# Kernel tuning notes

Measured on AMD Instinct MI355X. Metric: run time of the kernel, lower is better.

The kernel has to match this reference:

```python
import jax, jax.numpy as jnp
import numpy as np

B, T, N, P2, K_S = 8, 64, 128, 256, 64

def setup_inputs() -> dict:
    key = jax.random.key(0)
    k1, k2, k3, k4 = jax.random.split(key, 4)
    x = jax.random.normal(k1, (B, T, N, P2), dtype=jnp.float32)
    W_Q = jax.random.uniform(k2, (P2, K_S), dtype=jnp.float32)
    W_K = jax.random.uniform(k3, (P2, K_S), dtype=jnp.float32)
    W_V = jax.random.uniform(k4, (P2, P2), dtype=jnp.float32)
    return {"x": x, "W_Q": W_Q, "W_K": W_K, "W_V": W_V}

def reference(x, W_Q, W_K, W_V):
    # x: [B, T, N, P2]
    q = jnp.einsum('btnp,pk->btnk', x, W_Q)          # [B,T,N,K_S]
    k = jnp.einsum('btnp,pk->btnk', x, W_K)          # [B,T,N,K_S]
    v = jnp.einsum('btnp,pq->btnq', x, W_V)          # [B,T,N,P2]
    scale = jnp.sqrt(jnp.asarray(K_S, dtype=x.dtype))
    scores = jnp.einsum('btik,btjk->btij', q, k) / scale  # [B,T,N,N]
    # NOTE: original uses nn.Softmax(dim=1) -> softmax over the T axis.
    attn = jax.nn.softmax(scores, axis=1)
    return jnp.einsum('btij,btjq->btiq', attn, v)    # [B,T,N,P2]
```

## Files before the change

### kernel.cpp

```cpp
#include <hip/hip_runtime.h>
#include <hip/hip_bf16.h>

#define Bv 8
#define Tv 64
#define Nv 128
#define P2v 256
#define KSv 64

typedef __attribute__((ext_vector_type(8))) short bf8;
typedef __attribute__((ext_vector_type(4))) float f4;

#define MFMA16(a, b, c) __builtin_amdgcn_mfma_f32_16x16x32_bf16((a), (b), (c), 0, 0, 0)

union B8U {
  bf8 v;
  short s[8];
};

__device__ __forceinline__ unsigned short f2bf(float f) {
  unsigned u = __float_as_uint(f);
  return (unsigned short)((u + 0x7fffu + ((u >> 16) & 1u)) >> 16);
}
__device__ __forceinline__ float bf2f(unsigned short h) {
  return __uint_as_float(((unsigned)h) << 16);
}

__device__ __forceinline__ int qswz(int i, int ks) {
  int gin = ks >> 3;
  return i * 64 + ((gin ^ (i & 7)) << 3) + (ks & 7);
}
__device__ __forceinline__ int vswz(int q, int j) {
  int gin = j >> 3;
  return q * 128 + ((gin ^ (q & 7)) << 3) + (j & 7);
}

__global__ __launch_bounds__(256) void prep_w_kernel(
    const float* __restrict__ Wq, const float* __restrict__ Wk,
    const float* __restrict__ Wv, unsigned short* __restrict__ wqh,
    unsigned short* __restrict__ wql, unsigned short* __restrict__ wkh,
    unsigned short* __restrict__ wkl, unsigned short* __restrict__ wvf) {
  const int e = blockIdx.x * 256 + threadIdx.x;
  if (e < 32768) {
    const float* W = (e < 16384) ? Wq : Wk;
    unsigned short* oh = (e < 16384) ? wqh : wkh;
    unsigned short* ol = (e < 16384) ? wql : wkl;
    const int t = e & 16383;
    const int jj = t & 7, lane = (t >> 3) & 63, nt = (t >> 9) & 3, pt = t >> 11;
    const int p = pt * 32 + 8 * (lane >> 4) + jj;
    const int n = nt * 16 + (lane & 15);
    const float v = W[p * KSv + n];
    const unsigned short h = f2bf(v);
    oh[t] = h;
    ol[t] = f2bf(v - bf2f(h));
  } else {
    const int t = e - 32768;
    const int jj = t & 7, lane = (t >> 3) & 63, nt = (t >> 9) & 15, pt = t >> 13;
    const int p = pt * 32 + 8 * (lane >> 4) + jj;
    const int q = nt * 16 + (lane & 15);
    wvf[t] = f2bf(Wv[p * P2v + q]);
  }
}

__global__ __launch_bounds__(512) void qk_kernel(
    const float* __restrict__ x, const unsigned short* __restrict__ wqh,
    const unsigned short* __restrict__ wql,
    const unsigned short* __restrict__ wkh,
    const unsigned short* __restrict__ wkl, float* __restrict__ S) {
  __shared__ alignas(16) unsigned short qh_l[Nv * KSv];
  __shared__ alignas(16) unsigned short ql_l[Nv * KSv];
  __shared__ alignas(16) unsigned short kh_l[Nv * KSv];
  __shared__ alignas(16) unsigned short kl_l[Nv * KSv];
  const int bt = blockIdx.x;
  const float* __restrict__ X = x + (size_t)bt * (Nv * P2v);
  const int tid = threadIdx.x, lane = tid & 63, wid = tid >> 6;
  const int lg = lane >> 4, lr = lane & 15;
  const int r0 = wid * 16;

  const f4 zero = {0.f, 0.f, 0.f, 0.f};
  f4 aQ[4], aK[4];
#pragma unroll
  for (int n = 0; n < 4; ++n) {
    aQ[n] = zero;
    aK[n] = zero;
  }

  for (int kt = 0; kt < 8; ++kt) {
    const float* xr = X + (r0 + lr) * P2v + kt * 32 + lg * 8;
    const float4 x0 = *(const float4*)(xr);
    const float4 x1 = *(const float4*)(xr + 4);
    const float xs[8] = {x0.x, x0.y, x0.z, x0.w, x1.x, x1.y, x1.z, x1.w};
    B8U xh, xl;
#pragma unroll
    for (int j = 0; j < 8; ++j) {
      const unsigned short h = f2bf(xs[j]);
      xh.s[j] = (short)h;
      xl.s[j] = (short)f2bf(xs[j] - bf2f(h));
    }
#pragma unroll
    for (int n = 0; n < 4; ++n) {
      const int o = ((kt * 4 + n) * 64 + lane) * 8;
      const bf8 fqh = *(const bf8*)(wqh + o);
      const bf8 fql = *(const bf8*)(wql + o);
      const bf8 fkh = *(const bf8*)(wkh + o);
      const bf8 fkl = *(const bf8*)(wkl + o);
      aQ[n] = MFMA16(xh.v, fqh, aQ[n]);
      aQ[n] = MFMA16(xh.v, fql, aQ[n]);
      aQ[n] = MFMA16(xl.v, fqh, aQ[n]);
      aK[n] = MFMA16(xh.v, fkh, aK[n]);
      aK[n] = MFMA16(xh.v, fkl, aK[n]);
      aK[n] = MFMA16(xl.v, fkh, aK[n]);
    }
  }

#pragma unroll
  for (int n = 0; n < 4; ++n) {
#pragma unroll
    for (int r = 0; r < 4; ++r) {
      const int i = r0 + 4 * lg + r;
      const int ks = n * 16 + lr;
      const int off = qswz(i, ks);
      const float qv = aQ[n][r], kv = aK[n][r];
      const unsigned short qh = f2bf(qv), kh = f2bf(kv);
      qh_l[off] = qh;
      ql_l[off] = f2bf(qv - bf2f(qh));
      kh_l[off] = kh;
      kl_l[off] = f2bf(kv - bf2f(kh));
    }
  }
  __syncthreads();

  f4 aS[8];
#pragma unroll
  for (int n = 0; n < 8; ++n) aS[n] = zero;
#pragma unroll
  for (int kt = 0; kt < 2; ++kt) {
    const int qoff = qswz(r0 + lr, kt * 32 + lg * 8);
    const bf8 fqh = *(const bf8*)(qh_l + qoff);
    const bf8 fql = *(const bf8*)(ql_l + qoff);
#pragma unroll
    for (int n = 0; n < 8; ++n) {
      const int koff = qswz(n * 16 + lr, kt * 32 + lg * 8);
      const bf8 fkh = *(const bf8*)(kh_l + koff);
      const bf8 fkl = *(const bf8*)(kl_l + koff);
      aS[n] = MFMA16(fqh, fkh, aS[n]);
      aS[n] = MFMA16(fqh, fkl, aS[n]);
      aS[n] = MFMA16(fql, fkh, aS[n]);
    }
  }
  float* __restrict__ Sb = S + (size_t)bt * (Nv * Nv);
#pragma unroll
  for (int n = 0; n < 8; ++n) {
#pragma unroll
    for (int r = 0; r < 4; ++r) {
      Sb[(r0 + 4 * lg + r) * Nv + n * 16 + lr] = aS[n][r] * 0.125f;
    }
  }
}

__global__ __launch_bounds__(256) void softmax_t_kernel(float* __restrict__ S) {
  const int idx = blockIdx.x * 256 + threadIdx.x;
  const int j = idx & (Nv - 1);
  const int i = (idx >> 7) & (Nv - 1);
  const int b = idx >> 14;
  const size_t base = ((size_t)b * Tv * Nv * Nv) + (size_t)i * Nv + j;

  float vals[Tv];
  float m = -1e30f;
#pragma unroll
  for (int t = 0; t < Tv; ++t) {
    const float v = S[base + (size_t)t * Nv * Nv];
    vals[t] = v;
    m = fmaxf(m, v);
  }
  float s = 0.f;
#pragma unroll
  for (int t = 0; t < Tv; ++t) {
    const float e = __expf(vals[t] - m);
    vals[t] = e;
    s += e;
  }
  const float inv = 1.f / s;
#pragma unroll
  for (int t = 0; t < Tv; ++t) {
    S[base + (size_t)t * Nv * Nv] = vals[t] * inv;
  }
}

__global__ __launch_bounds__(512) void av_kernel(
    const float* __restrict__ x, const unsigned short* __restrict__ wvf,
    const float* __restrict__ A, float* __restrict__ out) {
  __shared__ alignas(16) unsigned short vt[P2v * Nv];
  const int bt = blockIdx.x;
  const float* __restrict__ X = x + (size_t)bt * (Nv * P2v);
  const float* __restrict__ Ab = A + (size_t)bt * (Nv * Nv);
  float* __restrict__ ob = out + (size_t)bt * (Nv * P2v);
  const int tid = threadIdx.x, lane = tid & 63, wid = tid >> 6;
  const int lg = lane >> 4, lr = lane & 15;
  const int r0 = wid * 16;

  const f4 zero = {0.f, 0.f, 0.f, 0.f};
  f4 aV[16];
#pragma unroll
  for (int n = 0; n < 16; ++n) aV[n] = zero;

  for (int kt = 0; kt < 8; ++kt) {
    const float* xr = X + (r0 + lr) * P2v + kt * 32 + lg * 8;
    const float4 x0 = *(const float4*)(xr);
    const float4 x1 = *(const float4*)(xr + 4);
    const float xs[8] = {x0.x, x0.y, x0.z, x0.w, x1.x, x1.y, x1.z, x1.w};
    B8U xh;
#pragma unroll
    for (int j = 0; j < 8; ++j) xh.s[j] = (short)f2bf(xs[j]);
#pragma unroll
    for (int n = 0; n < 16; ++n) {
      const int o = ((kt * 16 + n) * 64 + lane) * 8;
      const bf8 wv = *(const bf8*)(wvf + o);
      aV[n] = MFMA16(xh.v, wv, aV[n]);
    }
  }
#pragma unroll
  for (int n = 0; n < 16; ++n) {
#pragma unroll
    for (int r = 0; r < 4; ++r) {
      const int q = n * 16 + lr;
      const int j = r0 + 4 * lg + r;
      vt[vswz(q, j)] = f2bf(aV[n][r]);
    }
  }
  __syncthreads();

  f4 aO[16];
#pragma unroll
  for (int n = 0; n < 16; ++n) aO[n] = zero;
  for (int kt = 0; kt < 4; ++kt) {
    const float* ar = Ab + (r0 + lr) * Nv + kt * 32 + lg * 8;
    const float4 a0 = *(const float4*)(ar);
    const float4 a1 = *(const float4*)(ar + 4);
    const float as_[8] = {a0.x, a0.y, a0.z, a0.w, a1.x, a1.y, a1.z, a1.w};
    B8U af;
#pragma unroll
    for (int j = 0; j < 8; ++j) af.s[j] = (short)f2bf(as_[j]);
#pragma unroll
    for (int n = 0; n < 16; ++n) {
      const int voff = vswz(n * 16 + lr, kt * 32 + lg * 8);
      const bf8 vf = *(const bf8*)(vt + voff);
      aO[n] = MFMA16(af.v, vf, aO[n]);
    }
  }
#pragma unroll
  for (int n = 0; n < 16; ++n) {
#pragma unroll
    for (int r = 0; r < 4; ++r) {
      ob[(r0 + 4 * lg + r) * P2v + n * 16 + lr] = aO[n][r];
    }
  }
}

extern "C" void kernel_launch(void* const* d_in, const int* in_sizes, int n_in,
                              void* d_out, int out_size, void* d_ws,
                              size_t ws_size, hipStream_t stream) {
  const float* x = (const float*)d_in[0];
  const float* Wq = (const float*)d_in[1];
  const float* Wk = (const float*)d_in[2];
  const float* Wv = (const float*)d_in[3];
  float* out = (float*)d_out;

  unsigned short* wqh = (unsigned short*)d_ws;
  unsigned short* wql = wqh + 16384;
  unsigned short* wkh = wql + 16384;
  unsigned short* wkl = wkh + 16384;
  unsigned short* wvf = wkl + 16384;
  float* S = (float*)((char*)d_ws + 262144);

  hipLaunchKernelGGL(prep_w_kernel, dim3(384), dim3(256), 0, stream, Wq, Wk,
                     Wv, wqh, wql, wkh, wkl, wvf);
  hipLaunchKernelGGL(qk_kernel, dim3(Bv * Tv), dim3(512), 0, stream, x, wqh,
                     wql, wkh, wkl, S);
  hipLaunchKernelGGL(softmax_t_kernel, dim3(Bv * Nv * Nv / 256), dim3(256), 0,
                     stream, S);
  hipLaunchKernelGGL(av_kernel, dim3(Bv * Tv), dim3(512), 0, stream, x, wvf, S,
                     out);
}
```

Baseline: 89.21 us.

## Fuse V projection into QK kernel and stage V through workspace

Adds a qkv_kernel that computes Q, K and V from a single read of x, writing V as transposed bf16 to a workspace buffer. A new av_stage_kernel loads that precomputed V into shared memory instead of recomputing the projection from x. This path runs only when the workspace is large enough; otherwise the old kernels run with partial unrolling and packed ushort4 stores to shared memory. The intent is to avoid reading x twice and to shorten the AV kernel, at the cost of a 32MB V round trip through global memory and higher register pressure in the fused kernel.

Result: slower. 144.9 us (+62.5%).

```diff
diff --git a/kernel.cpp b/kernel.cpp
--- a/kernel.cpp
+++ b/kernel.cpp
@@ -61,6 +61,205 @@
   }
 }
 
+__global__ __launch_bounds__(512) void qkv_kernel(
+    const float* __restrict__ x, const unsigned short* __restrict__ wqh,
+    const unsigned short* __restrict__ wql,
+    const unsigned short* __restrict__ wkh,
+    const unsigned short* __restrict__ wkl,
+    const unsigned short* __restrict__ wvf, float* __restrict__ S,
+    unsigned short* __restrict__ Vt) {
+  __shared__ alignas(16) unsigned short qh_l[Nv * KSv];
+  __shared__ alignas(16) unsigned short ql_l[Nv * KSv];
+  __shared__ alignas(16) unsigned short kh_l[Nv * KSv];
+  __shared__ alignas(16) unsigned short kl_l[Nv * KSv];
+  const int bt = blockIdx.x;
+  const float* __restrict__ X = x + (size_t)bt * (Nv * P2v);
+  const int tid = threadIdx.x, lane = tid & 63, wid = tid >> 6;
+  const int lg = lane >> 4, lr = lane & 15;
+  const int r0 = wid * 16;
+
+  const f4 zero = {0.f, 0.f, 0.f, 0.f};
+  f4 aQ[4], aK[4], aV[16];
+#pragma unroll
+  for (int n = 0; n < 4; ++n) {
+    aQ[n] = zero;
+    aK[n] = zero;
+  }
+#pragma unroll
+  for (int n = 0; n < 16; ++n) aV[n] = zero;
+
+#pragma unroll 2
+  for (int kt = 0; kt < 8; ++kt) {
+    const float* xr = X + (r0 + lr) * P2v + kt * 32 + lg * 8;
+    const float4 x0 = *(const float4*)(xr);
+    const float4 x1 = *(const float4*)(xr + 4);
+    const float xs[8] = {x0.x, x0.y, x0.z, x0.w, x1.x, x1.y, x1.z, x1.w};
+    B8U xh, xl;
+#pragma unroll
+    for (int j = 0; j < 8; ++j) {
+      const unsigned short h = f2bf(xs[j]);
+      xh.s[j] = (short)h;
+      xl.s[j] = (short)f2bf(xs[j] - bf2f(h));
+    }
+#pragma unroll
+    for (int n = 0; n < 4; ++n) {
+      const int o = ((kt * 4 + n) * 64 + lane) * 8;
+      const bf8 fqh = *(const bf8*)(wqh + o);
+      const bf8 fql = *(const bf8*)(wql + o);
+      const bf8 fkh = *(const bf8*)(wkh + o);
+      const bf8 fkl = *(const bf8*)(wkl + o);
+      aQ[n] = MFMA16(xh.v, fqh, aQ[n]);
+      aQ[n] = MFMA16(xh.v, fql, aQ[n]);
+      aQ[n] = MFMA16(xl.v, fqh, aQ[n]);
+      aK[n] = MFMA16(xh.v, fkh, aK[n]);
+      aK[n] = MFMA16(xh.v, fkl, aK[n]);
+      aK[n] = MFMA16(xl.v, fkh, aK[n]);
+    }
+#pragma unroll
+    for (int n = 0; n < 16; ++n) {
+      const int o = ((kt * 16 + n) * 64 + lane) * 8;
+      const bf8 wv = *(const bf8*)(wvf + o);
+      aV[n] = MFMA16(xh.v, wv, aV[n]);
+    }
+  }
+
+  unsigned short* __restrict__ Vtb = Vt + (size_t)bt * (P2v * Nv);
+  const int j0 = r0 + 4 * lg;
+#pragma unroll
+  for (int n = 0; n < 16; ++n) {
+    const int q = n * 16 + lr;
+    ushort4 pk;
+    pk.x = f2bf(aV[n][0]);
+    pk.y = f2bf(aV[n][1]);
+    pk.z = f2bf(aV[n][2]);
+    pk.w = f2bf(aV[n][3]);
+    *(ushort4*)(Vtb + q * Nv + j0) = pk;
+  }
+
+#pragma unroll
+  for (int n = 0; n < 4; ++n) {
+#pragma unroll
+    for (int r = 0; r < 4; ++r) {
+      const int i = r0 + 4 * lg + r;
+      const int ks = n * 16 + lr;
+      const int off = qswz(i, ks);
+      const float qv = aQ[n][r], kv = aK[n][r];
+      const unsigned short qh = f2bf(qv), kh = f2bf(kv);
+      qh_l[off] = qh;
+      ql_l[off] = f2bf(qv - bf2f(qh));
+      kh_l[off] = kh;
+      kl_l[off] = f2bf(kv - bf2f(kh));
+    }
+  }
+  __syncthreads();
+
+  f4 aS[8];
+#pragma unroll
+  for (int n = 0; n < 8; ++n) aS[n] = zero;
+#pragma unroll
+  for (int kt = 0; kt < 2; ++kt) {
+    const int qoff = qswz(r0 + lr, kt * 32 + lg * 8);
+    const bf8 fqh = *(const bf8*)(qh_l + qoff);
+    const bf8 fql = *(const bf8*)(ql_l + qoff);
+#pragma unroll
+    for (int n = 0; n < 8; ++n) {
+      const int koff = qswz(n * 16 + lr, kt * 32 + lg * 8);
+      const bf8 fkh = *(const bf8*)(kh_l + koff);
+      const bf8 fkl = *(const bf8*)(kl_l + koff);
+      aS[n] = MFMA16(fqh, fkh, aS[n]);
+      aS[n] = MFMA16(fqh, fkl, aS[n]);
+      aS[n] = MFMA16(fql, fkh, aS[n]);
+    }
+  }
+  float* __restrict__ Sb = S + (size_t)bt * (Nv * Nv);
+#pragma unroll
+  for (int n = 0; n < 8; ++n) {
+#pragma unroll
+    for (int r = 0; r < 4; ++r) {
+      Sb[(r0 + 4 * lg + r) * Nv + n * 16 + lr] = aS[n][r] * 0.125f;
+    }
+  }
+}
+
+__global__ __launch_bounds__(256) void softmax_t_kernel(float* __restrict__ S) {
+  const int idx = blockIdx.x * 256 + threadIdx.x;
+  const int j = idx & (Nv - 1);
+  const int i = (idx >> 7) & (Nv - 1);
+  const int b = idx >> 14;
+  const size_t base = ((size_t)b * Tv * Nv * Nv) + (size_t)i * Nv + j;
+
+  float vals[Tv];
+  float m = -1e30f;
+#pragma unroll
+  for (int t = 0; t < Tv; ++t) {
+    const float v = S[base + (size_t)t * Nv * Nv];
+    vals[t] = v;
+    m = fmaxf(m, v);
+  }
+  float s = 0.f;
+#pragma unroll
+  for (int t = 0; t < Tv; ++t) {
+    const float e = __expf(vals[t] - m);
+    vals[t] = e;
+    s += e;
+  }
+  const float inv = 1.f / s;
+#pragma unroll
+  for (int t = 0; t < Tv; ++t) {
+    S[base + (size_t)t * Nv * Nv] = vals[t] * inv;
+  }
+}
+
+__global__ __launch_bounds__(512) void av_stage_kernel(
+    const float* __restrict__ A, const unsigned short* __restrict__ Vt,
+    float* __restrict__ out) {
+  __shared__ alignas(16) unsigned short vt[P2v * Nv];
+  const int bt = blockIdx.x;
+  const float* __restrict__ Ab = A + (size_t)bt * (Nv * Nv);
+  const unsigned short* __restrict__ Vtb = Vt + (size_t)bt * (P2v * Nv);
+  float* __restrict__ ob = out + (size_t)bt * (Nv * P2v);
+  const int tid = threadIdx.x, lane = tid & 63, wid = tid >> 6;
+  const int lg = lane >> 4, lr = lane & 15;
+  const int r0 = wid * 16;
+
+#pragma unroll
+  for (int it = 0; it < 8; ++it) {
+    const int c = it * 512 + tid;
+    const int q = c >> 4, gin = c & 15;
+    const uint4 v = *(const uint4*)(Vtb + c * 8);
+    *(uint4*)(vt + q * Nv + ((gin ^ (q & 7)) << 3)) = v;
+  }
+  __syncthreads();
+
+  const f4 zero = {0.f, 0.f, 0.f, 0.f};
+  f4 aO[16];
+#pragma unroll
+  for (int n = 0; n < 16; ++n) aO[n] = zero;
+#pragma unroll
+  for (int kt = 0; kt < 4; ++kt) {
+    const float* ar = Ab + (r0 + lr) * Nv + kt * 32 + lg * 8;
+    const float4 a0 = *(const float4*)(ar);
+    const float4 a1 = *(const float4*)(ar + 4);
+    const float as_[8] = {a0.x, a0.y, a0.z, a0.w, a1.x, a1.y, a1.z, a1.w};
+    B8U af;
+#pragma unroll
+    for (int j = 0; j < 8; ++j) af.s[j] = (short)f2bf(as_[j]);
+#pragma unroll
+    for (int n = 0; n < 16; ++n) {
+      const int voff = vswz(n * 16 + lr, kt * 32 + lg * 8);
+      const bf8 vf = *(const bf8*)(vt + voff);
+      aO[n] = MFMA16(af.v, vf, aO[n]);
+    }
+  }
+#pragma unroll
+  for (int n = 0; n < 16; ++n) {
+#pragma unroll
+    for (int r = 0; r < 4; ++r) {
+      ob[(r0 + 4 * lg + r) * P2v + n * 16 + lr] = aO[n][r];
+    }
+  }
+}
+
 __global__ __launch_bounds__(512) void qk_kernel(
     const float* __restrict__ x, const unsigned short* __restrict__ wqh,
     const unsigned short* __restrict__ wql,
@@ -83,7 +282,7 @@
     aQ[n] = zero;
     aK[n] = zero;
   }
-
+#pragma unroll 2
   for (int kt = 0; kt < 8; ++kt) {
     const float* xr = X + (r0 + lr) * P2v + kt * 32 + lg * 8;
     const float4 x0 = *(const float4*)(xr);
@@ -111,7 +310,6 @@
       aK[n] = MFMA16(xl.v, fkh, aK[n]);
     }
   }
-
 #pragma unroll
   for (int n = 0; n < 4; ++n) {
 #pragma unroll
@@ -128,7 +326,6 @@
     }
   }
   __syncthreads();
-
   f4 aS[8];
 #pragma unroll
   for (int n = 0; n < 8; ++n) aS[n] = zero;
@@ -154,35 +351,6 @@
     for (int r = 0; r < 4; ++r) {
       Sb[(r0 + 4 * lg + r) * Nv + n * 16 + lr] = aS[n][r] * 0.125f;
     }
-  }
-}
-
-__global__ __launch_bounds__(256) void softmax_t_kernel(float* __restrict__ S) {
-  const int idx = blockIdx.x * 256 + threadIdx.x;
-  const int j = idx & (Nv - 1);
-  const int i = (idx >> 7) & (Nv - 1);
-  const int b = idx >> 14;
-  const size_t base = ((size_t)b * Tv * Nv * Nv) + (size_t)i * Nv + j;
-
-  float vals[Tv];
-  float m = -1e30f;
-#pragma unroll
-  for (int t = 0; t < Tv; ++t) {
-    const float v = S[base + (size_t)t * Nv * Nv];
-    vals[t] = v;
-    m = fmaxf(m, v);
-  }
-  float s = 0.f;
-#pragma unroll
-  for (int t = 0; t < Tv; ++t) {
-    const float e = __expf(vals[t] - m);
-    vals[t] = e;
-    s += e;
-  }
-  const float inv = 1.f / s;
-#pragma unroll
-  for (int t = 0; t < Tv; ++t) {
-    S[base + (size_t)t * Nv * Nv] = vals[t] * inv;
   }
 }
 
@@ -202,7 +370,7 @@
   f4 aV[16];
 #pragma unroll
   for (int n = 0; n < 16; ++n) aV[n] = zero;
-
+#pragma unroll 2
   for (int kt = 0; kt < 8; ++kt) {
     const float* xr = X + (r0 + lr) * P2v + kt * 32 + lg * 8;
     const float4 x0 = *(const float4*)(xr);
@@ -218,20 +386,23 @@
       aV[n] = MFMA16(xh.v, wv, aV[n]);
     }
   }
+  const int j0 = r0 + 4 * lg;
 #pragma unroll
   for (int n = 0; n < 16; ++n) {
-#pragma unroll
-    for (int r = 0; r < 4; ++r) {
-      const int q = n * 16 + lr;
-      const int j = r0 + 4 * lg + r;
-      vt[vswz(q, j)] = f2bf(aV[n][r]);
-    }
+    const int q = n * 16 + lr;
+    ushort4 pk;
+    pk.x = f2bf(aV[n][0]);
+    pk.y = f2bf(aV[n][1]);
+    pk.z = f2bf(aV[n][2]);
+    pk.w = f2bf(aV[n][3]);
+    *(ushort4*)(vt + vswz(q, j0)) = pk;
   }
   __syncthreads();
 
   f4 aO[16];
 #pragma unroll
   for (int n = 0; n < 16; ++n) aO[n] = zero;
+#pragma unroll
   for (int kt = 0; kt < 4; ++kt) {
     const float* ar = Ab + (r0 + lr) * Nv + kt * 32 + lg * 8;
     const float4 a0 = *(const float4*)(ar);
@@ -271,13 +442,24 @@
   unsigned short* wkl = wkh + 16384;
   unsigned short* wvf = wkl + 16384;
   float* S = (float*)((char*)d_ws + 262144);
+  unsigned short* Vt = (unsigned short*)((char*)d_ws + 262144 + 33554432);
+  const size_t need_big = 262144ull + 33554432ull + 33554432ull;
 
   hipLaunchKernelGGL(prep_w_kernel, dim3(384), dim3(256), 0, stream, Wq, Wk,
                      Wv, wqh, wql, wkh, wkl, wvf);
-  hipLaunchKernelGGL(qk_kernel, dim3(Bv * Tv), dim3(512), 0, stream, x, wqh,
-                     wql, wkh, wkl, S);
-  hipLaunchKernelGGL(softmax_t_kernel, dim3(Bv * Nv * Nv / 256), dim3(256), 0,
-                     stream, S);
-  hipLaunchKernelGGL(av_kernel, dim3(Bv * Tv), dim3(512), 0, stream, x, wvf, S,
-                     out);
-}
+  if (ws_size >= need_big) {
+    hipLaunchKernelGGL(qkv_kernel, dim3(Bv * Tv), dim3(512), 0, stream, x, wqh,
+                       wql, wkh, wkl, wvf, S, Vt);
+    hipLaunchKernelGGL(softmax_t_kernel, dim3(Bv * Nv * Nv / 256), dim3(256),
+                       0, stream, S);
+    hipLaunchKernelGGL(av_stage_kernel, dim3(Bv * Tv), dim3(512), 0, stream, S,
+                       Vt, out);
+  } else {
+    hipLaunchKernelGGL(qk_kernel, dim3(Bv * Tv), dim3(512), 0, stream, x, wqh,
+                       wql, wkh, wkl, S);
+    hipLaunchKernelGGL(softmax_t_kernel, dim3(Bv * Nv * Nv / 256), dim3(256),
+                       0, stream, S);
+    hipLaunchKernelGGL(av_kernel, dim3(Bv * Tv), dim3(512), 0, stream, x, wvf,
+                       S, out);
+  }
+}
```

## Stage x tiles in LDS and store softmax output as bf16

Applied to the files above, without the earlier changes.

The QK and AV kernels now stage x in shared memory as swizzled bf16 chunks. Each wave owns one weight column tile and loops over all row tiles, so weight fragments are loaded once per wave and reused across rows, where before each wave reloaded all weight tiles. Softmax writes attention probabilities as bf16 into a separate workspace buffer, halving the traffic for the AV read. AV now computes its output in two halves to reduce LDS use. The cost is extra block syncs and LDS round trips.

Result: faster. 86.35 us (-3.2%).

```diff
diff --git a/kernel.cpp b/kernel.cpp
--- a/kernel.cpp
+++ b/kernel.cpp
@@ -12,11 +12,6 @@
 
 #define MFMA16(a, b, c) __builtin_amdgcn_mfma_f32_16x16x32_bf16((a), (b), (c), 0, 0, 0)
 
-union B8U {
-  bf8 v;
-  short s[8];
-};
-
 __device__ __forceinline__ unsigned short f2bf(float f) {
   unsigned u = __float_as_uint(f);
   return (unsigned short)((u + 0x7fffu + ((u >> 16) & 1u)) >> 16);
@@ -25,13 +20,11 @@
   return __uint_as_float(((unsigned)h) << 16);
 }
 
-__device__ __forceinline__ int qswz(int i, int ks) {
-  int gin = ks >> 3;
-  return i * 64 + ((gin ^ (i & 7)) << 3) + (ks & 7);
-}
-__device__ __forceinline__ int vswz(int q, int j) {
-  int gin = j >> 3;
-  return q * 128 + ((gin ^ (q & 7)) << 3) + (j & 7);
+__device__ __forceinline__ int swz64(int r, int c) {
+  return r * 64 + ((((c >> 3)) ^ (r & 7)) << 3) + (c & 7);
+}
+__device__ __forceinline__ int swz128(int r, int c) {
+  return r * 128 + ((((c >> 3)) ^ (r & 7)) << 3) + (c & 7);
 }
 
 __global__ __launch_bounds__(256) void prep_w_kernel(
@@ -66,6 +59,8 @@
     const unsigned short* __restrict__ wql,
     const unsigned short* __restrict__ wkh,
     const unsigned short* __restrict__ wkl, float* __restrict__ S) {
+  __shared__ alignas(16) unsigned short xh_l[Nv * KSv];
+  __shared__ alignas(16) unsigned short xl_l[Nv * KSv];
   __shared__ alignas(16) unsigned short qh_l[Nv * KSv];
   __shared__ alignas(16) unsigned short ql_l[Nv * KSv];
   __shared__ alignas(16) unsigned short kh_l[Nv * KSv];
@@ -74,72 +69,82 @@
   const float* __restrict__ X = x + (size_t)bt * (Nv * P2v);
   const int tid = threadIdx.x, lane = tid & 63, wid = tid >> 6;
   const int lg = lane >> 4, lr = lane & 15;
+  const bool isQ = (wid < 4);
+  const int nt = wid & 3;
+  const unsigned short* __restrict__ wh = isQ ? wqh : wkh;
+  const unsigned short* __restrict__ wl = isQ ? wql : wkl;
+
+  const f4 zero = {0.f, 0.f, 0.f, 0.f};
+  f4 acc[8];
+#pragma unroll
+  for (int rt = 0; rt < 8; ++rt) acc[rt] = zero;
+
+  const int srow = tid >> 4;
+  const int sp = (tid & 15) * 4;
+
+  for (int c = 0; c < 4; ++c) {
+    __syncthreads();
+#pragma unroll
+    for (int pass = 0; pass < 4; ++pass) {
+      const int row = srow + pass * 32;
+      const float4 v = *(const float4*)(X + row * P2v + c * 64 + sp);
+      ushort4 h, l;
+      h.x = f2bf(v.x); l.x = f2bf(v.x - bf2f(h.x));
+      h.y = f2bf(v.y); l.y = f2bf(v.y - bf2f(h.y));
+      h.z = f2bf(v.z); l.z = f2bf(v.z - bf2f(h.z));
+      h.w = f2bf(v.w); l.w = f2bf(v.w - bf2f(h.w));
+      const int off = swz64(row, sp);
+      *(ushort4*)(xh_l + off) = h;
+      *(ushort4*)(xl_l + off) = l;
+    }
+    __syncthreads();
+#pragma unroll
+    for (int ktl = 0; ktl < 2; ++ktl) {
+      const int kt = c * 2 + ktl;
+      const int o = ((kt * 4 + nt) * 64 + lane) * 8;
+      const bf8 fh = *(const bf8*)(wh + o);
+      const bf8 fl = *(const bf8*)(wl + o);
+#pragma unroll
+      for (int rt = 0; rt < 8; ++rt) {
+        const int xoff = swz64(rt * 16 + lr, ktl * 32 + lg * 8);
+        const bf8 xh = *(const bf8*)(xh_l + xoff);
+        const bf8 xl = *(const bf8*)(xl_l + xoff);
+        acc[rt] = MFMA16(xh, fh, acc[rt]);
+        acc[rt] = MFMA16(xh, fl, acc[rt]);
+        acc[rt] = MFMA16(xl, fh, acc[rt]);
+      }
+    }
+  }
+
+  unsigned short* const oh = isQ ? qh_l : kh_l;
+  unsigned short* const ol = isQ ? ql_l : kl_l;
+#pragma unroll
+  for (int rt = 0; rt < 8; ++rt) {
+#pragma unroll
+    for (int rr = 0; rr < 4; ++rr) {
+      const int i = rt * 16 + 4 * lg + rr;
+      const int ks = nt * 16 + lr;
+      const int off = swz64(i, ks);
+      const float v = acc[rt][rr];
+      const unsigned short h = f2bf(v);
+      oh[off] = h;
+      ol[off] = f2bf(v - bf2f(h));
+    }
+  }
+  __syncthreads();
+
   const int r0 = wid * 16;
-
-  const f4 zero = {0.f, 0.f, 0.f, 0.f};
-  f4 aQ[4], aK[4];
-#pragma unroll
-  for (int n = 0; n < 4; ++n) {
-    aQ[n] = zero;
-    aK[n] = zero;
-  }
-
-  for (int kt = 0; kt < 8; ++kt) {
-    const float* xr = X + (r0 + lr) * P2v + kt * 32 + lg * 8;
-    const float4 x0 = *(const float4*)(xr);
-    const float4 x1 = *(const float4*)(xr + 4);
-    const float xs[8] = {x0.x, x0.y, x0.z, x0.w, x1.x, x1.y, x1.z, x1.w};
-    B8U xh, xl;
-#pragma unroll
-    for (int j = 0; j < 8; ++j) {
-      const unsigned short h = f2bf(xs[j]);
-      xh.s[j] = (short)h;
-      xl.s[j] = (short)f2bf(xs[j] - bf2f(h));
-    }
-#pragma unroll
-    for (int n = 0; n < 4; ++n) {
-      const int o = ((kt * 4 + n) * 64 + lane) * 8;
-      const bf8 fqh = *(const bf8*)(wqh + o);
-      const bf8 fql = *(const bf8*)(wql + o);
-      const bf8 fkh = *(const bf8*)(wkh + o);
-      const bf8 fkl = *(const bf8*)(wkl + o);
-      aQ[n] = MFMA16(xh.v, fqh, aQ[n]);
-      aQ[n] = MFMA16(xh.v, fql, aQ[n]);
-      aQ[n] = MFMA16(xl.v, fqh, aQ[n]);
-      aK[n] = MFMA16(xh.v, fkh, aK[n]);
-      aK[n] = MFMA16(xh.v, fkl, aK[n]);
-      aK[n] = MFMA16(xl.v, fkh, aK[n]);
-    }
-  }
-
-#pragma unroll
-  for (int n = 0; n < 4; ++n) {
-#pragma unroll
-    for (int r = 0; r < 4; ++r) {
-      const int i = r0 + 4 * lg + r;
-      const int ks = n * 16 + lr;
-      const int off = qswz(i, ks);
-      const float qv = aQ[n][r], kv = aK[n][r];
-      const unsigned short qh = f2bf(qv), kh = f2bf(kv);
-      qh_l[off] = qh;
-      ql_l[off] = f2bf(qv - bf2f(qh));
-      kh_l[off] = kh;
-      kl_l[off] = f2bf(kv - bf2f(kh));
-    }
-  }
-  __syncthreads();
-
   f4 aS[8];
 #pragma unroll
   for (int n = 0; n < 8; ++n) aS[n] = zero;
 #pragma unroll
-  for (int kt = 0; kt < 2; ++kt) {
-    const int qoff = qswz(r0 + lr, kt * 32 + lg * 8);
+  for (int kt2 = 0; kt2 < 2; ++kt2) {
+    const int qoff = swz64(r0 + lr, kt2 * 32 + lg * 8);
     const bf8 fqh = *(const bf8*)(qh_l + qoff);
     const bf8 fql = *(const bf8*)(ql_l + qoff);
 #pragma unroll
     for (int n = 0; n < 8; ++n) {
-      const int koff = qswz(n * 16 + lr, kt * 32 + lg * 8);
+      const int koff = swz64(n * 16 + lr, kt2 * 32 + lg * 8);
       const bf8 fkh = *(const bf8*)(kh_l + koff);
       const bf8 fkl = *(const bf8*)(kl_l + koff);
       aS[n] = MFMA16(fqh, fkh, aS[n]);
@@ -151,13 +156,14 @@
 #pragma unroll
   for (int n = 0; n < 8; ++n) {
 #pragma unroll
-    for (int r = 0; r < 4; ++r) {
-      Sb[(r0 + 4 * lg + r) * Nv + n * 16 + lr] = aS[n][r] * 0.125f;
-    }
-  }
-}
-
-__global__ __launch_bounds__(256) void softmax_t_kernel(float* __restrict__ S) {
+    for (int rr = 0; rr < 4; ++rr) {
+      Sb[(r0 + 4 * lg + rr) * Nv + n * 16 + lr] = aS[n][rr] * 0.125f;
+    }
+  }
+}
+
+__global__ __launch_bounds__(256) void softmax_t_kernel(
+    const float* __restrict__ S, unsigned short* __restrict__ Abf) {
   const int idx = blockIdx.x * 256 + threadIdx.x;
   const int j = idx & (Nv - 1);
   const int i = (idx >> 7) & (Nv - 1);
@@ -182,76 +188,103 @@
   const float inv = 1.f / s;
 #pragma unroll
   for (int t = 0; t < Tv; ++t) {
-    S[base + (size_t)t * Nv * Nv] = vals[t] * inv;
+    Abf[base + (size_t)t * Nv * Nv] = f2bf(vals[t] * inv);
   }
 }
 
 __global__ __launch_bounds__(512) void av_kernel(
     const float* __restrict__ x, const unsigned short* __restrict__ wvf,
-    const float* __restrict__ A, float* __restrict__ out) {
-  __shared__ alignas(16) unsigned short vt[P2v * Nv];
+    const unsigned short* __restrict__ Abf, float* __restrict__ out) {
+  __shared__ alignas(16) unsigned short xa[Nv * KSv];
+  __shared__ alignas(16) unsigned short vth[Nv * Nv];
   const int bt = blockIdx.x;
   const float* __restrict__ X = x + (size_t)bt * (Nv * P2v);
-  const float* __restrict__ Ab = A + (size_t)bt * (Nv * Nv);
+  const unsigned short* __restrict__ Ab = Abf + (size_t)bt * (Nv * Nv);
   float* __restrict__ ob = out + (size_t)bt * (Nv * P2v);
   const int tid = threadIdx.x, lane = tid & 63, wid = tid >> 6;
   const int lg = lane >> 4, lr = lane & 15;
   const int r0 = wid * 16;
 
+  bf8 af[4];
+#pragma unroll
+  for (int kt = 0; kt < 4; ++kt) {
+    af[kt] = *(const bf8*)(Ab + (r0 + lr) * Nv + kt * 32 + lg * 8);
+  }
+
   const f4 zero = {0.f, 0.f, 0.f, 0.f};
   f4 aV[16];
 #pragma unroll
   for (int n = 0; n < 16; ++n) aV[n] = zero;
 
-  for (int kt = 0; kt < 8; ++kt) {
-    const float* xr = X + (r0 + lr) * P2v + kt * 32 + lg * 8;
-    const float4 x0 = *(const float4*)(xr);
-    const float4 x1 = *(const float4*)(xr + 4);
-    const float xs[8] = {x0.x, x0.y, x0.z, x0.w, x1.x, x1.y, x1.z, x1.w};
-    B8U xh;
-#pragma unroll
-    for (int j = 0; j < 8; ++j) xh.s[j] = (short)f2bf(xs[j]);
-#pragma unroll
-    for (int n = 0; n < 16; ++n) {
-      const int o = ((kt * 16 + n) * 64 + lane) * 8;
-      const bf8 wv = *(const bf8*)(wvf + o);
-      aV[n] = MFMA16(xh.v, wv, aV[n]);
-    }
-  }
-#pragma unroll
-  for (int n = 0; n < 16; ++n) {
-#pragma unroll
-    for (int r = 0; r < 4; ++r) {
-      const int q = n * 16 + lr;
-      const int j = r0 + 4 * lg + r;
-      vt[vswz(q, j)] = f2bf(aV[n][r]);
-    }
-  }
-  __syncthreads();
-
-  f4 aO[16];
-#pragma unroll
-  for (int n = 0; n < 16; ++n) aO[n] = zero;
-  for (int kt = 0; kt < 4; ++kt) {
-    const float* ar = Ab + (r0 + lr) * Nv + kt * 32 + lg * 8;
-    const float4 a0 = *(const float4*)(ar);
-    const float4 a1 = *(const float4*)(ar + 4);
-    const float as_[8] = {a0.x, a0.y, a0.z, a0.w, a1.x, a1.y, a1.z, a1.w};
-    B8U af;
-#pragma unroll
-    for (int j = 0; j < 8; ++j) af.s[j] = (short)f2bf(as_[j]);
-#pragma unroll
-    for (int n = 0; n < 16; ++n) {
-      const int voff = vswz(n * 16 + lr, kt * 32 + lg * 8);
-      const bf8 vf = *(const bf8*)(vt + voff);
-      aO[n] = MFMA16(af.v, vf, aO[n]);
-    }
-  }
-#pragma unroll
-  for (int n = 0; n < 16; ++n) {
-#pragma unroll
-    for (int r = 0; r < 4; ++r) {
-      ob[(r0 + 4 * lg + r) * P2v + n * 16 + lr] = aO[n][r];
+  const int srow = tid >> 4;
+  const int sp = (tid & 15) * 4;
+
+  for (int c = 0; c < 4; ++c) {
+    __syncthreads();
+#pragma unroll
+    for (int pass = 0; pass < 4; ++pass) {
+      const int row = srow + pass * 32;
+      const float4 v = *(const float4*)(X + row * P2v + c * 64 + sp);
+      ushort4 h;
+      h.x = f2bf(v.x);
+      h.y = f2bf(v.y);
+      h.z = f2bf(v.z);
+      h.w = f2bf(v.w);
+      *(ushort4*)(xa + swz64(row, sp)) = h;
+    }
+    __syncthreads();
+#pragma unroll
+    for (int ktl = 0; ktl < 2; ++ktl) {
+      const int kt = c * 2 + ktl;
+#pragma unroll
+      for (int h = 0; h < 2; ++h) {
+        const int ntile = h * 8 + wid;
+        const int o = ((kt * 16 + ntile) * 64 + lane) * 8;
+        const bf8 fv = *(const bf8*)(wvf + o);
+#pragma unroll
+        for (int rt = 0; rt < 8; ++rt) {
+          const bf8 xh =
+              *(const bf8*)(xa + swz64(rt * 16 + lr, ktl * 32 + lg * 8));
+          aV[h * 8 + rt] = MFMA16(xh, fv, aV[h * 8 + rt]);
+        }
+      }
+    }
+  }
+
+#pragma unroll
+  for (int h = 0; h < 2; ++h) {
+    if (h == 1) __syncthreads();
+    const int ql = wid * 16 + lr;
+#pragma unroll
+    for (int rt = 0; rt < 8; ++rt) {
+      const int j0 = rt * 16 + 4 * lg;
+      ushort4 pk;
+      pk.x = f2bf(aV[h * 8 + rt][0]);
+      pk.y = f2bf(aV[h * 8 + rt][1]);
+      pk.z = f2bf(aV[h * 8 + rt][2]);
+      pk.w = f2bf(aV[h * 8 + rt][3]);
+      *(ushort4*)(vth + swz128(ql, j0)) = pk;
+    }
+    __syncthreads();
+
+    f4 aO[8];
+#pragma unroll
+    for (int n = 0; n < 8; ++n) aO[n] = zero;
+#pragma unroll
+    for (int kt = 0; kt < 4; ++kt) {
+#pragma unroll
+      for (int n = 0; n < 8; ++n) {
+        const bf8 vf =
+            *(const bf8*)(vth + swz128(n * 16 + lr, kt * 32 + lg * 8));
+        aO[n] = MFMA16(af[kt], vf, aO[n]);
+      }
+    }
+#pragma unroll
+    for (int n = 0; n < 8; ++n) {
+#pragma unroll
+      for (int rr = 0; rr < 4; ++rr) {
+        ob[(r0 + 4 * lg + rr) * P2v + h * 128 + n * 16 + lr] = aO[n][rr];
+      }
     }
   }
 }
@@ -271,13 +304,14 @@
   unsigned short* wkl = wkh + 16384;
   unsigned short* wvf = wkl + 16384;
   float* S = (float*)((char*)d_ws + 262144);
+  unsigned short* Abf = (unsigned short*)((char*)d_ws + 262144 + 33554432);
 
   hipLaunchKernelGGL(prep_w_kernel, dim3(384), dim3(256), 0, stream, Wq, Wk,
                      Wv, wqh, wql, wkh, wkl, wvf);
   hipLaunchKernelGGL(qk_kernel, dim3(Bv * Tv), dim3(512), 0, stream, x, wqh,
                      wql, wkh, wkl, S);
   hipLaunchKernelGGL(softmax_t_kernel, dim3(Bv * Nv * Nv / 256), dim3(256), 0,
-                     stream, S);
-  hipLaunchKernelGGL(av_kernel, dim3(Bv * Tv), dim3(512), 0, stream, x, wvf, S,
-                     out);
-}
+                     stream, S, Abf);
+  hipLaunchKernelGGL(av_kernel, dim3(Bv * Tv), dim3(512), 0, stream, x, wvf,
+                     Abf, out);
+}
```
